# Optimization experiments

Hardware: AMD Instinct MI355X
Metric: run time of the kernel (lower is better)

The kernel has to match this reference:

```python
import jax, jax.numpy as jnp
import numpy as np

OUTPUT_SIZE = 200
IOU_THRESHOLD = 0.5
SCORE_THRESHOLD = 0.01


def setup_inputs() -> dict:
    key = jax.random.key(0)
    k1, k2, k3 = jax.random.split(key, 3)
    B, N, C = 8, 2048, 80
    # well-formed boxes in [0,1]: (min_xy, max_xy)
    centers = jax.random.uniform(k1, (B, N, 2))
    sizes = jax.random.uniform(k2, (B, N, 2), minval=0.02, maxval=0.3)
    boxes = jnp.concatenate([centers - sizes / 2, centers + sizes / 2], axis=-1)
    scores = jax.random.uniform(k3, (B, N, C))
    x = jnp.concatenate([boxes, scores], axis=-1)  # [B, N, 4+C]
    return {"x": x}


def _box_iou(b):
    # b: [N, 4] (x1, y1, x2, y2) -> [N, N] IoU
    lt = jnp.maximum(b[:, None, :2], b[None, :, :2])
    rb = jnp.minimum(b[:, None, 2:], b[None, :, 2:])
    wh = jnp.maximum(rb - lt, 0.0)
    inter = wh[..., 0] * wh[..., 1]
    area = (b[:, 2] - b[:, 0]) * (b[:, 3] - b[:, 1])
    union = area[:, None] + area[None, :] - inter
    return inter / jnp.maximum(union, 1e-8)


def _nms_one_class(iou_b, scores_bc):
    # iou_b: [N, N] (shared across classes), scores_bc: [N]
    N = scores_bc.shape[0]
    order = jnp.argsort(-scores_bc)            # descending score order
    s_sorted = scores_bc[order]
    keep0 = s_sorted > SCORE_THRESHOLD
    pos = jnp.arange(N)

    def body(i, keep):
        row = iou_b[order[i]][order]           # IoU of i-th ranked box vs all, in sorted order
        sup = keep[i]                          # only a kept box suppresses others
        return keep & ~((row > IOU_THRESHOLD) & (pos > i) & sup)

    keep = jax.lax.fori_loop(0, N, body, keep0)
    # cap to max_output_size_per_class: keep only first OUTPUT_SIZE kept boxes
    rank = jnp.cumsum(keep.astype(jnp.int32))
    keep = keep & (rank <= OUTPUT_SIZE)
    sel_scores = jnp.where(keep, s_sorted, -jnp.inf)
    return sel_scores, order


def _combined_nms_one_batch(boxes_b, scores_b, iou_b):
    # boxes_b: [N,4], scores_b: [N,C], iou_b: [N,N]
    N, C = scores_b.shape
    sel_scores, order = jax.vmap(_nms_one_class, in_axes=(None, 1))(iou_b, scores_b)  # [C,N] each
    flat_scores = sel_scores.reshape(C * N)
    top_scores, top_idx = jax.lax.top_k(flat_scores, OUTPUT_SIZE)  # global top across classes
    cls = top_idx // N
    pos = top_idx % N
    box_idx = order[cls, pos]                  # original box indices
    top_boxes = jnp.clip(boxes_b[box_idx], 0.0, 1.0)  # clip_boxes=True
    valid = jnp.isfinite(top_scores)
    out = jnp.concatenate([
        cls.astype(jnp.float32)[:, None],
        top_scores[:, None],
        top_boxes,
    ], axis=-1)                                # [OUTPUT_SIZE, 6] = (cls, score, x1, y1, x2, y2)
    return jnp.where(valid[:, None], out, 0.0)


def reference(x):
    boxes = x[..., :4]                         # [B, N, 4]
    scores = x[..., 4:]                        # [B, N, C]
    iou = jax.vmap(_box_iou)(boxes)            # [B, N, N] (boxes shared across classes)
    return jax.vmap(_combined_nms_one_batch)(boxes, scores, iou)  # [B, OUTPUT_SIZE, 6]
```

## Files before the change

### kernel.cpp

```cpp
#include <hip/hip_runtime.h>
#include <stdint.h>

typedef unsigned long long u64;
typedef unsigned int u32;

#define NB 8
#define NN 2048
#define NC 80
#define ROW 84
#define OUT_K 200
#define IOU_T 0.5f
#define SCORE_T 0.01f
#define TGT 896
#define POOL 1024

__device__ __forceinline__ void ce_desc(u64* a, int i, int j, int k) {
    u64 a0 = a[i], a1 = a[i + j];
    bool up = ((i & k) == 0);
    if (up ? (a0 < a1) : (a0 > a1)) { a[i] = a1; a[i + j] = a0; }
}

__device__ __forceinline__ void ceg(u64& x, u64& y, bool up) {
    u64 a0 = x, a1 = y;
    if (up ? (a0 < a1) : (a0 > a1)) { x = a1; y = a0; }
}

__device__ __forceinline__ void wave_rounds512(u64* a, int base, int k, int jhi, int lane) {
    for (int j = jhi; j > 0; j >>= 1) {
        #pragma unroll
        for (int p = 0; p < 4; p++) {
            int r = lane + p * 64;
            int low = r & (j - 1);
            int high = (r & ~(j - 1)) << 1;
            ce_desc(a, base + (high | low), j, k);
        }
        __builtin_amdgcn_wave_barrier();
    }
}

__device__ __forceinline__ void wave_rounds256(u64* a, int base, int k, int jhi, int lane) {
    for (int j = jhi; j > 0; j >>= 1) {
        #pragma unroll
        for (int p = 0; p < 2; p++) {
            int r = lane + p * 64;
            int low = r & (j - 1);
            int high = (r & ~(j - 1)) << 1;
            ce_desc(a, base + (high | low), j, k);
        }
        __builtin_amdgcn_wave_barrier();
    }
}

__device__ __forceinline__ void pair_merge256(u64* a, int base, int off, int lane) {
    #pragma unroll
    for (int p0 = 0; p0 < 4; p0++) {
        int p = lane + p0 * 64;
        u64 xv = a[base + p];
        u64 yv = a[base + off + 255 - p];
        a[base + p] = xv > yv ? xv : yv;
    }
    __builtin_amdgcn_wave_barrier();
    wave_rounds256(a, base, 0x40000000, 128, lane);
}

__device__ __forceinline__ void sort2048(u64* key, int tid, int lane, int wv) {
    const int base = wv * 512;
    for (int k = 2; k <= 512; k <<= 1)
        wave_rounds512(key, base, k, k >> 1, lane);
    __syncthreads();
    #pragma unroll
    for (int p = 0; p < 4; p++) {
        int r = tid + p * 256;
        int low = r & 511, high = (r & ~511) << 1;
        ce_desc(key, high | low, 512, 1024);
    }
    __syncthreads();
    wave_rounds512(key, base, 1024, 256, lane);
    __syncthreads();
    #pragma unroll
    for (int p = 0; p < 4; p++) {
        int r = tid + p * 256;
        int low = r & 1023, high = (r & ~1023) << 1;
        ce_desc(key, high | low, 1024, 2048);
    }
    __syncthreads();
    #pragma unroll
    for (int p = 0; p < 4; p++) {
        int r = tid + p * 256;
        int low = r & 511, high = (r & ~511) << 1;
        ce_desc(key, high | low, 512, 2048);
    }
    __syncthreads();
    wave_rounds512(key, base, 2048, 256, lane);
    __syncthreads();
}

__device__ __forceinline__ void sort1024(u64* a, int tid, int lane, int wv) {
    const int t4 = tid * 4;
    const int sb = wv * 256;
    {
        u64 v0 = a[t4], v1 = a[t4 + 1], v2 = a[t4 + 2], v3 = a[t4 + 3];
        ceg(v0, v1, true);
        ceg(v2, v3, false);
        const bool d4 = ((t4 & 4) == 0);
        ceg(v0, v2, d4); ceg(v1, v3, d4);
        ceg(v0, v1, d4); ceg(v2, v3, d4);
        a[t4] = v0; a[t4 + 1] = v1; a[t4 + 2] = v2; a[t4 + 3] = v3;
    }
    __builtin_amdgcn_wave_barrier();
    for (int k = 8; k <= 256; k <<= 1) {
        for (int j = k >> 1; j >= 4; j >>= 1) {
            #pragma unroll
            for (int p = 0; p < 2; p++) {
                int r = lane + p * 64;
                int low = r & (j - 1);
                int high = (r & ~(j - 1)) << 1;
                ce_desc(a, sb + (high | low), j, k);
            }
            __builtin_amdgcn_wave_barrier();
        }
        {
            u64 v0 = a[t4], v1 = a[t4 + 1], v2 = a[t4 + 2], v3 = a[t4 + 3];
            const bool d = ((t4 & k) == 0);
            ceg(v0, v2, d); ceg(v1, v3, d);
            ceg(v0, v1, d); ceg(v2, v3, d);
            a[t4] = v0; a[t4 + 1] = v1; a[t4 + 2] = v2; a[t4 + 3] = v3;
        }
        __builtin_amdgcn_wave_barrier();
    }
    __syncthreads();
    #pragma unroll
    for (int p = 0; p < 2; p++) {
        int r = tid + p * 256;
        int low = r & 255, high = (r & ~255) << 1;
        ce_desc(a, high | low, 256, 512);
    }
    __syncthreads();
    for (int j = 128; j >= 4; j >>= 1) {
        #pragma unroll
        for (int p = 0; p < 2; p++) {
            int r = lane + p * 64;
            int low = r & (j - 1);
            int high = (r & ~(j - 1)) << 1;
            ce_desc(a, sb + (high | low), j, 512);
        }
        __builtin_amdgcn_wave_barrier();
    }
    {
        u64 v0 = a[t4], v1 = a[t4 + 1], v2 = a[t4 + 2], v3 = a[t4 + 3];
        const bool d = ((t4 & 512) == 0);
        ceg(v0, v2, d); ceg(v1, v3, d);
        ceg(v0, v1, d); ceg(v2, v3, d);
        a[t4] = v0; a[t4 + 1] = v1; a[t4 + 2] = v2; a[t4 + 3] = v3;
    }
    __syncthreads();
    #pragma unroll
    for (int p = 0; p < 2; p++) {
        int r = tid + p * 256;
        int low = r & 511, high = (r & ~511) << 1;
        ce_desc(a, high | low, 512, 1024);
    }
    __syncthreads();
    #pragma unroll
    for (int p = 0; p < 2; p++) {
        int r = tid + p * 256;
        int low = r & 255, high = (r & ~255) << 1;
        ce_desc(a, high | low, 256, 1024);
    }
    __syncthreads();
    for (int j = 128; j >= 4; j >>= 1) {
        #pragma unroll
        for (int p = 0; p < 2; p++) {
            int r = lane + p * 64;
            int low = r & (j - 1);
            int high = (r & ~(j - 1)) << 1;
            ce_desc(a, sb + (high | low), j, 1024);
        }
        __builtin_amdgcn_wave_barrier();
    }
    {
        u64 v0 = a[t4], v1 = a[t4 + 1], v2 = a[t4 + 2], v3 = a[t4 + 3];
        const bool d = ((t4 & 1024) == 0);
        ceg(v0, v2, d); ceg(v1, v3, d);
        ceg(v0, v1, d); ceg(v2, v3, d);
        a[t4] = v0; a[t4 + 1] = v1; a[t4 + 2] = v2; a[t4 + 3] = v3;
    }
    __syncthreads();
}

__device__ __forceinline__ bool iou_gt_half(float4 a, float aa, float4 b, float ab) {
    float ltx = fmaxf(a.x, b.x);
    float lty = fmaxf(a.y, b.y);
    float rbx = fminf(a.z, b.z);
    float rby = fminf(a.w, b.w);
    float wd = fmaxf(__fsub_rn(rbx, ltx), 0.0f);
    float hd = fmaxf(__fsub_rn(rby, lty), 0.0f);
    float inter = __fmul_rn(wd, hd);
    float uni = __fsub_rn(__fadd_rn(aa, ab), inter);
    float m = fmaxf(uni, 1e-8f);
    float d2 = __fmul_rn(2.0f, inter);
    bool sup = d2 > m;
    if (sup && (__fsub_rn(d2, m) <= __fmul_rn(m, 1.2e-7f)))
        sup = __fdiv_rn(inter, m) > IOU_T;
    return sup;
}

__device__ __forceinline__ float bcast(float v, int sl) {
    return __int_as_float(__builtin_amdgcn_readlane(__float_as_int(v), sl));
}

__device__ __forceinline__ int greedy(const u64* cand, int maxch, const float* xb,
        float4* kept_box, float* kept_area, u64* kept_key,
        u64* s_sup, int* s_kept, int* s_done, int tid, int lane, int wv,
        int keptc_in) {
    if (tid == 0) { *s_kept = keptc_in; *s_done = 0; }
    __syncthreads();
    int keptc = keptc_in;
    for (int ch = 0; ch < maxch; ch++) {
        int n = ch * 64 + lane;
        u64 mykey = cand[n];
        float sc = __uint_as_float((u32)(mykey >> 32));
        bool valid = sc > SCORE_T;
        u64 vball = __ballot(valid);
        if (vball == 0ULL) break;

        u32 orig = 2047u - (u32)(mykey & 0x7FFu);
        float4 bx = *(const float4*)(xb + (size_t)orig * ROW);
        float ar = __fmul_rn(__fsub_rn(bx.z, bx.x), __fsub_rn(bx.w, bx.y));

        bool supA = false;
        int t = wv;
        for (; t + 12 < keptc; t += 16) {
            float4 kb0 = kept_box[t],     kb1 = kept_box[t + 4];
            float4 kb2 = kept_box[t + 8], kb3 = kept_box[t + 12];
            float ka0 = kept_area[t],     ka1 = kept_area[t + 4];
            float ka2 = kept_area[t + 8], ka3 = kept_area[t + 12];
            bool s0 = iou_gt_half(bx, ar, kb0, ka0);
            bool s1 = iou_gt_half(bx, ar, kb1, ka1);
            bool s2 = iou_gt_half(bx, ar, kb2, ka2);
            bool s3 = iou_gt_half(bx, ar, kb3, ka3);
            supA = supA | ((s0 | s1) | (s2 | s3));
        }
        for (; t < keptc; t += 4)
            supA = supA | iou_gt_half(bx, ar, kept_box[t], kept_area[t]);
        u64 supm = __ballot(supA);
        if (lane == 0) s_sup[wv] = supm;
        __syncthreads();

        if (wv == 0) {
            u64 alive = vball & ~s_sup[0] & ~s_sup[1] & ~s_sup[2] & ~s_sup[3];
            int kept = keptc;
            while (alive) {
                int bsel = (int)__builtin_ctzll(alive);
                if (lane == bsel) {
                    kept_key[kept] = mykey;
                    kept_box[kept] = bx;
                    kept_area[kept] = ar;
                }
                kept++;
                if (kept >= OUT_K) { *s_done = 1; break; }
                alive &= alive - 1;
                if (!alive) break;
                float4 pb = make_float4(bcast(bx.x, bsel), bcast(bx.y, bsel),
                                        bcast(bx.z, bsel), bcast(bx.w, bsel));
                float pa = bcast(ar, bsel);
                alive &= ~__ballot(iou_gt_half(bx, ar, pb, pa));
            }
            if (lane == 0) *s_kept = kept;
        }
        __syncthreads();
        keptc = *s_kept;
        if (*s_done) break;
        if (__popcll(vball) < 64) break;
    }
    __syncthreads();
    return keptc;
}

__global__ __launch_bounds__(256) void nms_kernel(
        const float* __restrict__ x, u64* __restrict__ cand_key) {
    const int bc = blockIdx.x;
    const int b = bc / NC;
    const int c = bc % NC;
    const int tid = threadIdx.x;
    const int lane = tid & 63;
    const int wv = tid >> 6;

    __shared__ __align__(16) u64 arr[2048];
    u64* comp = arr;
    u32* hist = (u32*)(arr + 1024);
    __shared__ float4 kept_box[OUT_K];
    __shared__ float kept_area[OUT_K];
    __shared__ u64 kept_key[OUT_K];
    __shared__ u64 s_sup[4];
    __shared__ u32 s_wsum[4];
    __shared__ u32 s_cnt, s_m;
    __shared__ int s_kept, s_done, s_thr;

    const float* xb = x + (size_t)b * NN * ROW;

    hist[tid] = 0;
    __syncthreads();
    float scv[8];
    #pragma unroll
    for (int w = 0; w < 8; w++) {
        int n = w * 256 + tid;
        float sc = xb[n * ROW + 4 + c];
        scv[w] = sc;
        int bin = (int)(sc * 256.0f); bin = bin > 255 ? 255 : bin;
        atomicAdd(&hist[bin], 1u);
    }
    __syncthreads();

    u32 cnt_mine = hist[tid];
    u32 incl = cnt_mine;
    #pragma unroll
    for (int off = 1; off < 64; off <<= 1) {
        u32 v = __shfl_down(incl, off, 64);
        if (lane + off < 64) incl += v;
    }
    if (lane == 0) s_wsum[wv] = incl;
    __syncthreads();
    u32 above = 0;
    #pragma unroll
    for (int w = 0; w < 4; w++) above += (w > wv) ? s_wsum[w] : 0;
    const u32 suf = incl + above;

    if (tid == 0) s_thr = 2;
    __syncthreads();
    if (suf >= TGT && suf - cnt_mine < TGT) s_thr = tid;
    __syncthreads();
    int t1 = s_thr;
    if (tid == t1) s_m = suf;
    __syncthreads();
    u32 m_tot = s_m;

    bool fb = (m_tot > POOL);
    int kept = 0;
    if (!fb) {
        if (tid == 0) s_cnt = 0;
        __syncthreads();
        #pragma unroll
        for (int w = 0; w < 8; w++) {
            float sc = scv[w];
            int bin = (int)(sc * 256.0f); bin = bin > 255 ? 255 : bin;
            if (bin >= t1) {
                int n = w * 256 + tid;
                u32 p = atomicAdd(&s_cnt, 1u);
                comp[p] = ((u64)__float_as_uint(sc) << 32) | (u64)(2047 - n);
            }
        }
        __syncthreads();
        for (int i = tid; i < POOL; i += 256) if (i >= (int)m_tot) comp[i] = 0ULL;
        __syncthreads();
        sort1024(comp, tid, lane, wv);
        kept = greedy(comp, POOL / 64, xb, kept_box, kept_area, kept_key,
                      s_sup, &s_kept, &s_done, tid, lane, wv, 0);

        while (kept < OUT_K && t1 > 2) {
            u32 T2 = m_tot + TGT;
            if (tid == 0) s_thr = 2;
            __syncthreads();
            if (suf >= T2 && suf - cnt_mine < T2) s_thr = tid;
            __syncthreads();
            int t2 = s_thr;
            if (tid == t2) s_m = suf;
            __syncthreads();
            u32 m2 = s_m;
            u32 size = m2 - m_tot;
            if (size == 0) break;
            if (size > POOL) { fb = true; break; }
            if (tid == 0) s_cnt = 0;
            __syncthreads();
            #pragma unroll
            for (int w = 0; w < 8; w++) {
                float sc = scv[w];
                int bin = (int)(sc * 256.0f); bin = bin > 255 ? 255 : bin;
                if (bin >= t2 && bin < t1) {
                    int n = w * 256 + tid;
                    u32 p = atomicAdd(&s_cnt, 1u);
                    comp[p] = ((u64)__float_as_uint(sc) << 32) | (u64)(2047 - n);
                }
            }
            __syncthreads();
            for (int i = tid; i < POOL; i += 256) if (i >= (int)size) comp[i] = 0ULL;
            __syncthreads();
            sort1024(comp, tid, lane, wv);
            kept = greedy(comp, POOL / 64, xb, kept_box, kept_area, kept_key,
                          s_sup, &s_kept, &s_done, tid, lane, wv, kept);
            m_tot = m2; t1 = t2;
        }
    }
    if (fb) {
        __syncthreads();
        #pragma unroll
        for (int w = 0; w < 8; w++) {
            int n = w * 256 + tid;
            arr[n] = ((u64)__float_as_uint(scv[w]) << 32) | (u64)(2047 - n);
        }
        __syncthreads();
        sort2048(arr, tid, lane, wv);
        kept = greedy(arr, 32, xb, kept_box, kept_area, kept_key,
                      s_sup, &s_kept, &s_done, tid, lane, wv, 0);
    }

    const int base_o = bc * OUT_K;
    if (tid < OUT_K) {
        u64 ok = 0ULL;
        if (tid < kept) {
            u64 kk = kept_key[tid];
            u32 flat = (u32)(c * OUT_K + tid);
            u32 orig = 2047u - (u32)(kk & 0x7FFu);
            ok = (kk & 0xFFFFFFFF00000000ULL) |
                 ((u64)(0x3FFFu - flat) << 11) | (u64)orig;
        }
        cand_key[base_o + tid] = ok;
    }
}

__global__ __launch_bounds__(256) void merge8_kernel(u64* __restrict__ cand_key) {
    const int blk = blockIdx.x;
    const int b = blk / 10;
    const int g = blk % 10;
    const int tid = threadIdx.x;
    const int lane = tid & 63;
    const int wv = tid >> 6;
    __shared__ __align__(16) u64 seg[2048];

    u64* src = cand_key + (size_t)(b * NC + g * 8) * OUT_K;

    #pragma unroll
    for (int q = 0; q < 8; q++) {
        seg[q * 256 + tid] = (tid < OUT_K) ? src[q * OUT_K + tid] : 0ULL;
    }
    __syncthreads();
    pair_merge256(seg, wv * 512, 256, lane);
    __syncthreads();
    if (wv < 2) pair_merge256(seg, wv * 1024, 512, lane);
    __syncthreads();
    if (wv == 0) pair_merge256(seg, 0, 1024, lane);
    __syncthreads();
    src[tid] = seg[tid];
}

__global__ __launch_bounds__(256) void final_kernel(
        const float* __restrict__ x, const u64* __restrict__ cand_key,
        float* __restrict__ out) {
    const int b = blockIdx.x;
    const int tid = threadIdx.x;
    const int lane = tid & 63;
    const int wv = tid >> 6;
    __shared__ __align__(16) u64 seg[2560];

    #pragma unroll
    for (int q = 0; q < 10; q++) {
        seg[q * 256 + tid] = cand_key[(size_t)(b * NC + q * 8) * OUT_K + tid];
    }
    __syncthreads();
    pair_merge256(seg, wv * 512, 256, lane);
    __syncthreads();
    if (wv == 0) pair_merge256(seg, 0, 512, lane);
    else if (wv == 1) pair_merge256(seg, 1024, 512, lane);
    else if (wv == 2) pair_merge256(seg, 2048, 256, lane);
    __syncthreads();
    if (wv == 0) pair_merge256(seg, 0, 1024, lane);
    __syncthreads();
    if (wv == 0) pair_merge256(seg, 0, 2048, lane);
    __syncthreads();

    const float* xb = x + (size_t)b * NN * ROW;
    if (tid < OUT_K) {
        u64 kk = seg[tid];
        float* o = out + ((size_t)b * OUT_K + tid) * 6;
        if (kk == 0ULL) {
            o[0] = 0.f; o[1] = 0.f; o[2] = 0.f; o[3] = 0.f; o[4] = 0.f; o[5] = 0.f;
        } else {
            u32 lo = (u32)(kk & 0xFFFFFFFFu);
            u32 flat = 0x3FFFu - ((lo >> 11) & 0x3FFFu);
            int cls = flat / OUT_K;
            u32 n = lo & 0x7FFu;
            float scf = __uint_as_float((u32)(kk >> 32));
            float4 bx = *(const float4*)(xb + (size_t)n * ROW);
            o[0] = (float)cls;
            o[1] = scf;
            o[2] = fminf(fmaxf(bx.x, 0.0f), 1.0f);
            o[3] = fminf(fmaxf(bx.y, 0.0f), 1.0f);
            o[4] = fminf(fmaxf(bx.z, 0.0f), 1.0f);
            o[5] = fminf(fmaxf(bx.w, 0.0f), 1.0f);
        }
    }
}

extern "C" void kernel_launch(void* const* d_in, const int* in_sizes, int n_in,
                              void* d_out, int out_size, void* d_ws, size_t ws_size,
                              hipStream_t stream) {
    const float* x = (const float*)d_in[0];
    float* out = (float*)d_out;
    u64* cand_key = (u64*)d_ws;
    nms_kernel<<<NB * NC, 256, 0, stream>>>(x, cand_key);
    merge8_kernel<<<NB * 10, 256, 0, stream>>>(cand_key);
    final_kernel<<<NB, 256, 0, stream>>>(x, cand_key, out);
}
```

Before: 163.3 us.

## Precompute intra-chunk IoU mask in wave 0 and prefetch candidate boxes to LDS

Wave 0 now builds a 64x64 intra-chunk suppression bitmask while waves 1-3 check candidates against already-kept boxes. The serial greedy loop then uses bit lookups from that mask instead of readlane broadcasts plus an IoU ballot, and kept entries are written in one pass by rank. Boxes and areas for the first 512 sorted candidates are gathered into shared memory up front so they are not fetched per chunk. In exchange, one fewer wave works on the kept-box checks, shared memory use grows, and wave 0 does 64 IoU evaluations per chunk.

```diff
diff --git a/kernel.cpp b/kernel.cpp
--- a/kernel.cpp
+++ b/kernel.cpp
@@ -205,11 +205,23 @@
     return sup;
 }
 
-__device__ __forceinline__ float bcast(float v, int sl) {
-    return __int_as_float(__builtin_amdgcn_readlane(__float_as_int(v), sl));
+__device__ __forceinline__ void prefetch512(const u64* cand, const float* xb,
+        float4* pbox, float* parea, int tid) {
+    #pragma unroll
+    for (int r = 0; r < 2; r++) {
+        int i = r * 256 + tid;
+        u64 k = cand[i];
+        u32 orig = 2047u - (u32)(k & 0x7FFu);
+        float4 bx = *(const float4*)(xb + (size_t)orig * ROW);
+        pbox[i] = bx;
+        parea[i] = __fmul_rn(__fsub_rn(bx.z, bx.x), __fsub_rn(bx.w, bx.y));
+    }
+    __syncthreads();
 }
 
 __device__ __forceinline__ int greedy(const u64* cand, int maxch, const float* xb,
+        const float4* pbox, const float* parea,
+        float4* s_cbox, float* s_car,
         float4* kept_box, float* kept_area, u64* kept_key,
         u64* s_sup, int* s_kept, int* s_done, int tid, int lane, int wv,
         int keptc_in) {
@@ -224,49 +236,72 @@
         u64 vball = __ballot(valid);
         if (vball == 0ULL) break;
 
-        u32 orig = 2047u - (u32)(mykey & 0x7FFu);
-        float4 bx = *(const float4*)(xb + (size_t)orig * ROW);
-        float ar = __fmul_rn(__fsub_rn(bx.z, bx.x), __fsub_rn(bx.w, bx.y));
-
-        bool supA = false;
-        int t = wv;
-        for (; t + 12 < keptc; t += 16) {
-            float4 kb0 = kept_box[t],     kb1 = kept_box[t + 4];
-            float4 kb2 = kept_box[t + 8], kb3 = kept_box[t + 12];
-            float ka0 = kept_area[t],     ka1 = kept_area[t + 4];
-            float ka2 = kept_area[t + 8], ka3 = kept_area[t + 12];
-            bool s0 = iou_gt_half(bx, ar, kb0, ka0);
-            bool s1 = iou_gt_half(bx, ar, kb1, ka1);
-            bool s2 = iou_gt_half(bx, ar, kb2, ka2);
-            bool s3 = iou_gt_half(bx, ar, kb3, ka3);
-            supA = supA | ((s0 | s1) | (s2 | s3));
-        }
-        for (; t < keptc; t += 4)
-            supA = supA | iou_gt_half(bx, ar, kept_box[t], kept_area[t]);
-        u64 supm = __ballot(supA);
-        if (lane == 0) s_sup[wv] = supm;
-        __syncthreads();
-
+        float4 bx; float ar;
+        const float4* cb; const float* ca;
+        if (ch < 8) {
+            bx = pbox[n];
+            ar = parea[n];
+            cb = pbox + ch * 64;
+            ca = parea + ch * 64;
+        } else {
+            u32 orig = 2047u - (u32)(mykey & 0x7FFu);
+            bx = *(const float4*)(xb + (size_t)orig * ROW);
+            ar = __fmul_rn(__fsub_rn(bx.z, bx.x), __fsub_rn(bx.w, bx.y));
+            if (wv == 0) { s_cbox[lane] = bx; s_car[lane] = ar; }
+            __builtin_amdgcn_wave_barrier();
+            cb = s_cbox; ca = s_car;
+        }
+
+        u64 colmask = 0ULL;
         if (wv == 0) {
-            u64 alive = vball & ~s_sup[0] & ~s_sup[1] & ~s_sup[2] & ~s_sup[3];
+            #pragma unroll 4
+            for (int j = 0; j < 64; j++) {
+                bool s = iou_gt_half(bx, ar, cb[j], ca[j]);
+                colmask |= ((u64)s) << j;
+            }
+        } else {
+            bool supA = false;
+            int t = wv - 1;
+            for (; t + 9 < keptc; t += 12) {
+                float4 kb0 = kept_box[t],     kb1 = kept_box[t + 3];
+                float4 kb2 = kept_box[t + 6], kb3 = kept_box[t + 9];
+                float ka0 = kept_area[t],     ka1 = kept_area[t + 3];
+                float ka2 = kept_area[t + 6], ka3 = kept_area[t + 9];
+                bool s0 = iou_gt_half(bx, ar, kb0, ka0);
+                bool s1 = iou_gt_half(bx, ar, kb1, ka1);
+                bool s2 = iou_gt_half(bx, ar, kb2, ka2);
+                bool s3 = iou_gt_half(bx, ar, kb3, ka3);
+                supA = supA | ((s0 | s1) | (s2 | s3));
+            }
+            for (; t < keptc; t += 3)
+                supA = supA | iou_gt_half(bx, ar, kept_box[t], kept_area[t]);
+            u64 supm = __ballot(supA);
+            if (lane == 0) s_sup[wv] = supm;
+        }
+        __syncthreads();
+
+        if (wv == 0) {
+            u64 alive = vball & ~s_sup[1] & ~s_sup[2] & ~s_sup[3];
             int kept = keptc;
+            u64 keptbits = 0ULL;
+            int donef = 0;
             while (alive) {
                 int bsel = (int)__builtin_ctzll(alive);
-                if (lane == bsel) {
-                    kept_key[kept] = mykey;
-                    kept_box[kept] = bx;
-                    kept_area[kept] = ar;
-                }
+                keptbits |= 1ULL << bsel;
                 kept++;
-                if (kept >= OUT_K) { *s_done = 1; break; }
+                if (kept >= OUT_K) { donef = 1; break; }
                 alive &= alive - 1;
                 if (!alive) break;
-                float4 pb = make_float4(bcast(bx.x, bsel), bcast(bx.y, bsel),
-                                        bcast(bx.z, bsel), bcast(bx.w, bsel));
-                float pa = bcast(ar, bsel);
-                alive &= ~__ballot(iou_gt_half(bx, ar, pb, pa));
-            }
-            if (lane == 0) *s_kept = kept;
+                alive &= ~__ballot(((colmask >> bsel) & 1ULL) != 0ULL);
+            }
+            u32 rank = (u32)__popcll(keptbits & ((1ULL << lane) - 1ULL));
+            if ((keptbits >> lane) & 1ULL) {
+                int idx = keptc + (int)rank;
+                kept_key[idx] = mykey;
+                kept_box[idx] = bx;
+                kept_area[idx] = ar;
+            }
+            if (lane == 0) { *s_kept = kept; if (donef) *s_done = 1; }
         }
         __syncthreads();
         keptc = *s_kept;
@@ -289,6 +324,10 @@
     __shared__ __align__(16) u64 arr[2048];
     u64* comp = arr;
     u32* hist = (u32*)(arr + 1024);
+    __shared__ __align__(16) float4 s_pbox[512];
+    __shared__ float s_parea[512];
+    __shared__ __align__(16) float4 s_cbox[64];
+    __shared__ float s_car[64];
     __shared__ float4 kept_box[OUT_K];
     __shared__ float kept_area[OUT_K];
     __shared__ u64 kept_key[OUT_K];
@@ -354,7 +393,9 @@
         for (int i = tid; i < POOL; i += 256) if (i >= (int)m_tot) comp[i] = 0ULL;
         __syncthreads();
         sort1024(comp, tid, lane, wv);
-        kept = greedy(comp, POOL / 64, xb, kept_box, kept_area, kept_key,
+        prefetch512(comp, xb, s_pbox, s_parea, tid);
+        kept = greedy(comp, POOL / 64, xb, s_pbox, s_parea, s_cbox, s_car,
+                      kept_box, kept_area, kept_key,
                       s_sup, &s_kept, &s_done, tid, lane, wv, 0);
 
         while (kept < OUT_K && t1 > 2) {
@@ -386,7 +427,9 @@
             for (int i = tid; i < POOL; i += 256) if (i >= (int)size) comp[i] = 0ULL;
             __syncthreads();
             sort1024(comp, tid, lane, wv);
-            kept = greedy(comp, POOL / 64, xb, kept_box, kept_area, kept_key,
+            prefetch512(comp, xb, s_pbox, s_parea, tid);
+            kept = greedy(comp, POOL / 64, xb, s_pbox, s_parea, s_cbox, s_car,
+                          kept_box, kept_area, kept_key,
                           s_sup, &s_kept, &s_done, tid, lane, wv, kept);
             m_tot = m2; t1 = t2;
         }
@@ -400,7 +443,9 @@
         }
         __syncthreads();
         sort2048(arr, tid, lane, wv);
-        kept = greedy(arr, 32, xb, kept_box, kept_area, kept_key,
+        prefetch512(arr, xb, s_pbox, s_parea, tid);
+        kept = greedy(arr, 32, xb, s_pbox, s_parea, s_cbox, s_car,
+                      kept_box, kept_area, kept_key,
                       s_sup, &s_kept, &s_done, tid, lane, wv, 0);
     }
 
```

Result: faster. 147.3 us (-9.8%).
